# Optimization experiments

Measured on AMD Instinct MI355X. Metric: run time of the kernel, lower is better.

Reference implementation:

```python
import jax, jax.numpy as jnp
import numpy as np

N_NODES = 100000
N_EDGES = 1600000
IN_DIM = 128
N_HID = 128


def setup_inputs() -> dict:
    key = jax.random.key(0)
    k1, k2, k3, k4 = jax.random.split(key, 4)
    node_feature = jax.random.normal(k1, (N_NODES, IN_DIM), dtype=jnp.float32)
    edge_index = jax.random.randint(k2, (2, N_EDGES), 0, N_NODES, dtype=jnp.int64)
    # GCN layer weights (glorot-ish scale)
    W1 = jax.random.normal(k3, (IN_DIM, N_HID), dtype=jnp.float32) / np.sqrt(IN_DIM)
    b1 = jnp.zeros((N_HID,), dtype=jnp.float32)
    W2 = jax.random.normal(k4, (N_HID, N_HID), dtype=jnp.float32) / np.sqrt(N_HID)
    b2 = jnp.zeros((N_HID,), dtype=jnp.float32)
    return {"node_feature": node_feature, "edge_index": edge_index,
            "W1": W1, "b1": b1, "W2": W2, "b2": b2}


def _gcn_layer(x, W, b, row, col, n_nodes):
    """GCNConv: x' = D^-1/2 (A + I) D^-1/2 (x W) + b, symmetric norm with self-loops."""
    xt = x @ W  # [N, out]
    ones = jnp.ones(row.shape[0], dtype=xt.dtype)
    deg = jnp.zeros((n_nodes,), dtype=xt.dtype).at[col].add(ones) + 1.0  # +1 self-loop
    dinv = jax.lax.rsqrt(deg)  # [N]
    norm = dinv[row] * dinv[col]  # [E]
    # gather messages from source (row), scatter-add into destination (col)
    agg = jnp.zeros_like(xt).at[col].add(xt[row] * norm[:, None])
    agg = agg + xt * (dinv * dinv)[:, None]  # self-loop contribution
    return agg + b


def reference(node_feature, edge_index, W1, b1, W2, b2):
    row, col = edge_index[0], edge_index[1]
    n = node_feature.shape[0]
    h = _gcn_layer(node_feature, W1, b1, row, col, n)
    # F.dropout with training=False is identity (eval-mode reference)
    h = _gcn_layer(h, W2, b2, row, col, n)
    return h
```

## Files before the change

### kernel.cpp

```cpp
#include <hip/hip_runtime.h>

typedef unsigned short ushort_t;
typedef __attribute__((ext_vector_type(8))) short short8;
typedef __attribute__((ext_vector_type(8))) unsigned short us8v;
typedef __attribute__((ext_vector_type(4))) float f32x4;

__device__ __forceinline__ float b2f(unsigned short u) {
    union { unsigned int i; float f; } v; v.i = ((unsigned int)u) << 16; return v.f;
}
__device__ __forceinline__ unsigned short f2b(float f) {
    union { float f; unsigned int i; } v; v.f = f;
    unsigned int r = (v.i + 0x7FFF + ((v.i >> 16) & 1)) >> 16;
    return (unsigned short)r;
}

__device__ __forceinline__ void load_edge(const int* __restrict__ ei, int e, int E,
                                          int is64, int& s, int& d) {
    if (is64) { s = ei[2 * e]; d = ei[2 * (E + e)]; }
    else      { s = ei[e];     d = ei[E + e]; }
}

__global__ void k_hist(const int* __restrict__ ei, int E, unsigned N,
                       int* __restrict__ bhist, int BSH, int NB) {
    __shared__ int lh[256];
    int t = threadIdx.x;
    for (int b = t; b < NB; b += 256) lh[b] = 0;
    int z = 0;
    for (int i = t; i < 512; i += 256) z |= ei[2 * i + 1];
    int is64 = (__syncthreads_or(z) == 0);
    int e0 = blockIdx.x * 4096;
    #pragma unroll
    for (int i = 0; i < 16; ++i) {
        int e = e0 + i * 256 + t;
        if (e < E) {
            int s, d; load_edge(ei, e, E, is64, s, d);
            if ((unsigned)s < N && (unsigned)d < N) atomicAdd(&lh[d >> BSH], 1);
        }
    }
    __syncthreads();
    for (int b = t; b < NB; b += 256) { int v = lh[b]; if (v) atomicAdd(&bhist[b], v); }
}

__global__ void k_scanb(const int* __restrict__ bhist, int NB,
                        int* __restrict__ bkbase, int* __restrict__ bkcur) {
    __shared__ int sd[256];
    int t = threadIdx.x;
    int v0 = (t < NB) ? bhist[t] : 0;
    sd[t] = v0;
    for (int o = 1; o < 256; o <<= 1) {
        __syncthreads();
        int v = (t >= o) ? sd[t - o] : 0;
        __syncthreads();
        sd[t] += v;
    }
    __syncthreads();
    if (t < NB) { int ex = sd[t] - v0; bkbase[t] = ex; bkcur[t] = ex; }
}

__global__ __launch_bounds__(256) void k_bucket(const int* __restrict__ ei, int E, unsigned N,
                                                int* __restrict__ bkcur,
                                                int* __restrict__ bs, int* __restrict__ bd,
                                                int BSH, int NB) {
    __shared__ int lss[4096];
    __shared__ int ldd[4096];
    __shared__ int lhist[256];
    __shared__ int lcur[256];
    int t = threadIdx.x;
    int e0 = blockIdx.x * 4096;
    for (int b = t; b < NB; b += 256) lhist[b] = 0;
    int z = 0;
    for (int i = t; i < 512; i += 256) z |= ei[2 * i + 1];
    int is64 = (__syncthreads_or(z) == 0);
    #pragma unroll
    for (int i = 0; i < 16; ++i) {
        int idx = i * 256 + t, e = e0 + idx;
        int s = -1, d = -1;
        if (e < E) {
            load_edge(ei, e, E, is64, s, d);
            if (!((unsigned)s < N && (unsigned)d < N)) d = -1;
        }
        lss[idx] = s; ldd[idx] = d;
        if (d >= 0) atomicAdd(&lhist[d >> BSH], 1);
    }
    __syncthreads();
    for (int b = t; b < NB; b += 256) {
        int v = lhist[b];
        lcur[b] = v ? atomicAdd(&bkcur[b], v) : 0;
    }
    __syncthreads();
    #pragma unroll
    for (int i = 0; i < 16; ++i) {
        int idx = i * 256 + t;
        int d = ldd[idx];
        if (d >= 0) {
            int p = atomicAdd(&lcur[d >> BSH], 1);
            bs[p] = lss[idx]; bd[p] = d;
        }
    }
}

__global__ void k_count2(const int* __restrict__ bd, const int* __restrict__ bkbase,
                         const int* __restrict__ bkcur, int N, int BSH,
                         int* __restrict__ cnt) {
    __shared__ int lc[512];
    int b = blockIdx.x, t = threadIdx.x;
    int nbase = b << BSH;
    int nn = min(1 << BSH, N - nbase);
    for (int j = t; j < nn; j += 256) lc[j] = 0;
    __syncthreads();
    int s0 = bkbase[b], s1 = bkcur[b];
    for (int i = s0 + t; i < s1; i += 256) atomicAdd(&lc[bd[i] - nbase], 1);
    __syncthreads();
    for (int j = t; j < nn; j += 256) cnt[nbase + j] = lc[j];
}

__global__ void k_assign(int* __restrict__ cnt, int N,
                         int* __restrict__ pos, float* __restrict__ dinv,
                         int* __restrict__ cursor, int* __restrict__ srcs,
                         int padidx) {
    __shared__ int sd[256];
    __shared__ int sbase;
    int t = threadIdx.x;
    int n = blockIdx.x * 256 + t;
    int c = (n < N) ? cnt[n] : 0;
    int cp = (c + 7) & ~7;
    sd[t] = cp;
    for (int o = 1; o < 256; o <<= 1) {
        __syncthreads();
        int v = (t >= o) ? sd[t - o] : 0;
        __syncthreads();
        sd[t] += v;
    }
    __syncthreads();
    if (t == 255) sbase = atomicAdd(cursor, sd[255]);
    __syncthreads();
    if (n < N) {
        int st = sbase + sd[t] - cp;
        pos[n] = st;
        dinv[n] = rsqrtf((float)c + 1.0f);
        cnt[n] = cp;
        for (int q = c; q < cp; ++q) srcs[st + q] = padidx;
    }
}

__global__ void k_fill2(const int* __restrict__ bs, const int* __restrict__ bd,
                        const int* __restrict__ bkbase, const int* __restrict__ bkcur,
                        const int* __restrict__ pos, int N, int BSH,
                        int* __restrict__ srcs) {
    __shared__ int lcur[512];
    int b = blockIdx.x, t = threadIdx.x;
    int nbase = b << BSH;
    int nn = min(1 << BSH, N - nbase);
    for (int j = t; j < nn; j += 256) lcur[j] = pos[nbase + j];
    __syncthreads();
    int s0 = bkbase[b], s1 = bkcur[b];
    for (int i = s0 + t; i < s1; i += 256) {
        int d = bd[i];
        int p = atomicAdd(&lcur[d - nbase], 1);
        srcs[p] = bs[i];
    }
}

__global__ void k_transpose(const float* __restrict__ W1, const float* __restrict__ W2,
                            ushort_t* __restrict__ WT, ushort_t* __restrict__ xt,
                            int N) {
    if (blockIdx.x == 2) {
        int t = threadIdx.x;
        if (t < 128) xt[((size_t)N << 7) + t] = 0;
        return;
    }
    const float* src = blockIdx.x ? W2 : W1;
    ushort_t* dst = WT + blockIdx.x * 16384;
    for (int i = threadIdx.x; i < 16384; i += 256) {
        int n = i >> 7, k = i & 127;
        dst[i] = f2b(src[k * 128 + n]);
    }
}

__global__ __launch_bounds__(256) void k_gemm(const float* __restrict__ A,
                                              const ushort_t* __restrict__ WT,
                                              ushort_t* __restrict__ C,
                                              const float* __restrict__ dinv, int M) {
    __shared__ __align__(16) ushort_t sA[64 * 136];
    __shared__ __align__(16) ushort_t sW[128 * 136];
    int t = threadIdx.x;
    int row0 = blockIdx.x * 64;

    #pragma unroll
    for (int it = 0; it < 8; ++it) {
        int flat = (it * 256 + t) * 8;
        int n = flat >> 7, k = flat & 127;
        uint4 v = *(const uint4*)(WT + flat);
        *(uint4*)(&sW[n * 136 + k]) = v;
    }
    #pragma unroll
    for (int it = 0; it < 4; ++it) {
        int flat = (it * 256 + t) * 8;
        int r = flat >> 7, cc = flat & 127;
        int row = row0 + r; if (row > M - 1) row = M - 1;
        const float* p = A + (size_t)row * 128 + cc;
        float4 f0 = *(const float4*)p;
        float4 f1 = *(const float4*)(p + 4);
        ushort_t tmp[8] __attribute__((aligned(16)));
        tmp[0] = f2b(f0.x); tmp[1] = f2b(f0.y); tmp[2] = f2b(f0.z); tmp[3] = f2b(f0.w);
        tmp[4] = f2b(f1.x); tmp[5] = f2b(f1.y); tmp[6] = f2b(f1.z); tmp[7] = f2b(f1.w);
        *(uint4*)(&sA[r * 136 + cc]) = *(const uint4*)tmp;
    }
    __syncthreads();

    int w = t >> 6, lane = t & 63;
    int m = lane & 15, quad = lane >> 4;

    f32x4 acc[8] = {};
    #pragma unroll
    for (int k0 = 0; k0 < 128; k0 += 32) {
        short8 af = *(const short8*)(&sA[(w * 16 + m) * 136 + k0 + quad * 8]);
        #pragma unroll
        for (int tt = 0; tt < 8; ++tt) {
            short8 bf = *(const short8*)(&sW[(tt * 16 + m) * 136 + k0 + quad * 8]);
            acc[tt] = __builtin_amdgcn_mfma_f32_16x16x32_bf16(af, bf, acc[tt], 0, 0, 0);
        }
    }
    #pragma unroll
    for (int r = 0; r < 4; ++r) {
        int row = row0 + w * 16 + quad * 4 + r;
        if (row < M) {
            float dd = dinv[row];
            #pragma unroll
            for (int tt = 0; tt < 8; ++tt)
                C[(size_t)row * 128 + tt * 16 + m] = f2b(dd * acc[tt][r]);
        }
    }
}

__global__ __launch_bounds__(256) void k_agg(const ushort_t* __restrict__ xt,
                                             const float* __restrict__ bias,
                                             float* __restrict__ out,
                                             const int* __restrict__ pos,
                                             const int* __restrict__ cnts,
                                             const float* __restrict__ dinv,
                                             const int* __restrict__ srcs, int N) {
    int lane = threadIdx.x & 63;
    int slot = lane >> 4, j = lane & 15;
    int d = (blockIdx.x << 2) + (threadIdx.x >> 6);
    if (d >= N) return;
    int cn = cnts[d];
    int start = pos[d];
    float dd = dinv[d];
    us8v vs = *(const us8v*)(xt + ((size_t)d << 7) + (j << 3));
    float4 bb0 = *(const float4*)(bias + (j << 3));
    float4 bb1 = *(const float4*)(bias + (j << 3) + 4);

    float a0 = 0.f, a1 = 0.f, a2 = 0.f, a3 = 0.f;
    float a4 = 0.f, a5 = 0.f, a6 = 0.f, a7 = 0.f;

    for (int base = 0; base < cn; base += 64) {
        int n = cn - base; if (n > 64) n = 64;
        int sv = 0;
        if (lane < n) sv = srcs[start + base + lane];
        #pragma unroll 2
        for (int c = 0; c < n; c += 8) {
            int s0 = __shfl(sv, c + slot);
            int s1 = __shfl(sv, c + 4 + slot);
            us8v v0 = *(const us8v*)(xt + ((size_t)s0 << 7) + (j << 3));
            us8v v1 = *(const us8v*)(xt + ((size_t)s1 << 7) + (j << 3));
            a0 += b2f(v0[0]); a1 += b2f(v0[1]); a2 += b2f(v0[2]); a3 += b2f(v0[3]);
            a4 += b2f(v0[4]); a5 += b2f(v0[5]); a6 += b2f(v0[6]); a7 += b2f(v0[7]);
            a0 += b2f(v1[0]); a1 += b2f(v1[1]); a2 += b2f(v1[2]); a3 += b2f(v1[3]);
            a4 += b2f(v1[4]); a5 += b2f(v1[5]); a6 += b2f(v1[6]); a7 += b2f(v1[7]);
        }
    }
    a0 += __shfl_xor(a0, 32); a1 += __shfl_xor(a1, 32);
    a2 += __shfl_xor(a2, 32); a3 += __shfl_xor(a3, 32);
    a4 += __shfl_xor(a4, 32); a5 += __shfl_xor(a5, 32);
    a6 += __shfl_xor(a6, 32); a7 += __shfl_xor(a7, 32);
    a0 += __shfl_xor(a0, 16); a1 += __shfl_xor(a1, 16);
    a2 += __shfl_xor(a2, 16); a3 += __shfl_xor(a3, 16);
    a4 += __shfl_xor(a4, 16); a5 += __shfl_xor(a5, 16);
    a6 += __shfl_xor(a6, 16); a7 += __shfl_xor(a7, 16);

    if (slot == 0) {
        float4 o0, o1;
        o0.x = dd * (a0 + b2f(vs[0])) + bb0.x;
        o0.y = dd * (a1 + b2f(vs[1])) + bb0.y;
        o0.z = dd * (a2 + b2f(vs[2])) + bb0.z;
        o0.w = dd * (a3 + b2f(vs[3])) + bb0.w;
        o1.x = dd * (a4 + b2f(vs[4])) + bb1.x;
        o1.y = dd * (a5 + b2f(vs[5])) + bb1.y;
        o1.z = dd * (a6 + b2f(vs[6])) + bb1.z;
        o1.w = dd * (a7 + b2f(vs[7])) + bb1.w;
        float4* po = (float4*)(out + ((size_t)d << 7) + (j << 3));
        po[0] = o0; po[1] = o1;
    }
}


extern "C" void kernel_launch(void* const* d_in, const int* in_sizes, int n_in,
                              void* d_out, int out_size, void* d_ws, size_t ws_size,
                              hipStream_t stream) {
    const float* x  = (const float*)d_in[0];
    const int*   ei = (const int*)d_in[1];
    const float* W1 = (const float*)d_in[2];
    const float* b1 = (const float*)d_in[3];
    const float* W2 = (const float*)d_in[4];
    const float* b2 = (const float*)d_in[5];
    float* out = (float*)d_out;

    const int N = in_sizes[0] / 128;
    const int E = in_sizes[1] / 2;

    int BSH = 9;
    int NB = (N + (1 << BSH) - 1) >> BSH;
    while (NB > 256) { BSH++; NB = (N + (1 << BSH) - 1) >> BSH; }

    char* ws = (char*)d_ws;
    size_t o = 0;
    auto take = [&](size_t bytes) { size_t r = o; o = (o + bytes + 255) & ~(size_t)255; return r; };
    size_t o_bhist  = take(256 * 4);
    size_t o_cursor = take(4);
    size_t zero_end = o;
    size_t o_bkbase = take(256 * 4);
    size_t o_bkcur  = take(256 * 4);
    size_t o_cnt    = take((size_t)N * 4);
    size_t o_pos    = take((size_t)N * 4);
    size_t o_dinv   = take((size_t)N * 4);
    size_t o_srcs   = take(((size_t)E + 7 * (size_t)N + 64) * 4);
    size_t o_WT     = take(2 * 128 * 128 * 2);
    size_t big_sz   = (size_t)E * 8 > (size_t)(N + 1) * 256 ? (size_t)E * 8
                                                            : (size_t)(N + 1) * 256;
    size_t o_big    = take(big_sz);
    (void)ws_size;

    int*      bhist  = (int*)(ws + o_bhist);
    int*      cursor = (int*)(ws + o_cursor);
    int*      bkbase = (int*)(ws + o_bkbase);
    int*      bkcur  = (int*)(ws + o_bkcur);
    int*      cnt    = (int*)(ws + o_cnt);
    int*      pos    = (int*)(ws + o_pos);
    float*    dinv   = (float*)(ws + o_dinv);
    int*      srcs   = (int*)(ws + o_srcs);
    ushort_t* WT     = (ushort_t*)(ws + o_WT);
    int*      bs     = (int*)(ws + o_big);
    int*      bd     = (int*)(ws + o_big) + E;
    ushort_t* xt     = (ushort_t*)(ws + o_big);
    float*    h      = out;

    hipMemsetAsync(d_ws, 0, zero_end, stream);

    int gE = (E + 4095) / 4096;
    int gN = (N + 255) / 256;
    k_hist<<<gE, 256, 0, stream>>>(ei, E, (unsigned)N, bhist, BSH, NB);
    k_scanb<<<1, 256, 0, stream>>>(bhist, NB, bkbase, bkcur);
    k_bucket<<<gE, 256, 0, stream>>>(ei, E, (unsigned)N, bkcur, bs, bd, BSH, NB);
    k_count2<<<NB, 256, 0, stream>>>(bd, bkbase, bkcur, N, BSH, cnt);
    k_assign<<<gN, 256, 0, stream>>>(cnt, N, pos, dinv, cursor, srcs, N);
    k_fill2<<<NB, 256, 0, stream>>>(bs, bd, bkbase, bkcur, pos, N, BSH, srcs);
    k_transpose<<<3, 256, 0, stream>>>(W1, W2, WT, xt, N);

    int gG = (N + 63) / 64;
    int gA = (N + 3) / 4;
    k_gemm<<<gG, 256, 0, stream>>>(x, WT, xt, dinv, N);
    k_agg<<<gA, 256, 0, stream>>>(xt, b1, h, pos, cnt, dinv, srcs, N);
    k_gemm<<<gG, 256, 0, stream>>>(h, WT + 16384, xt, dinv, N);
    k_agg<<<gA, 256, 0, stream>>>(xt, b2, out, pos, cnt, dinv, srcs, N);
}
```

Measured before the change: 352.5 us.

## Replace bucketed CSR build with direct atomics, store hidden layer as bf16

The two-level bucket sort (histogram, scan, bucket scatter, per-bucket count and fill) becomes a direct global-atomic degree count followed by a global-atomic fill into per-node cursors. This cuts the kernel launches and the intermediate bucket arrays, but adds contended global atomics and random writes. Separately, the first aggregation now writes its hidden output as bf16, which the second GEMM reads directly. That halves the intermediate traffic and drops a conversion in the GEMM. The aggregation loop is also reshaped to software-pipeline its gather loads.

```diff
diff --git a/kernel.cpp b/kernel.cpp
--- a/kernel.cpp
+++ b/kernel.cpp
@@ -16,108 +16,39 @@
 
 __device__ __forceinline__ void load_edge(const int* __restrict__ ei, int e, int E,
                                           int is64, int& s, int& d) {
-    if (is64) { s = ei[2 * e]; d = ei[2 * (E + e)]; }
-    else      { s = ei[e];     d = ei[E + e]; }
-}
-
-__global__ void k_hist(const int* __restrict__ ei, int E, unsigned N,
-                       int* __restrict__ bhist, int BSH, int NB) {
-    __shared__ int lh[256];
-    int t = threadIdx.x;
-    for (int b = t; b < NB; b += 256) lh[b] = 0;
+    if (is64) {
+        const long long* el = (const long long*)ei;
+        s = (int)el[e]; d = (int)el[E + e];
+    } else {
+        s = ei[e]; d = ei[E + e];
+    }
+}
+
+__device__ __forceinline__ int detect64(const int* __restrict__ ei, int t) {
     int z = 0;
     for (int i = t; i < 512; i += 256) z |= ei[2 * i + 1];
-    int is64 = (__syncthreads_or(z) == 0);
+    return (__syncthreads_or(z) == 0);
+}
+
+__global__ void k_count(const int* __restrict__ ei, int E, unsigned N,
+                        int* __restrict__ cnt) {
+    int t = threadIdx.x;
+    int is64 = detect64(ei, t);
     int e0 = blockIdx.x * 4096;
     #pragma unroll
     for (int i = 0; i < 16; ++i) {
         int e = e0 + i * 256 + t;
         if (e < E) {
             int s, d; load_edge(ei, e, E, is64, s, d);
-            if ((unsigned)s < N && (unsigned)d < N) atomicAdd(&lh[d >> BSH], 1);
-        }
-    }
-    __syncthreads();
-    for (int b = t; b < NB; b += 256) { int v = lh[b]; if (v) atomicAdd(&bhist[b], v); }
-}
-
-__global__ void k_scanb(const int* __restrict__ bhist, int NB,
-                        int* __restrict__ bkbase, int* __restrict__ bkcur) {
-    __shared__ int sd[256];
-    int t = threadIdx.x;
-    int v0 = (t < NB) ? bhist[t] : 0;
-    sd[t] = v0;
-    for (int o = 1; o < 256; o <<= 1) {
-        __syncthreads();
-        int v = (t >= o) ? sd[t - o] : 0;
-        __syncthreads();
-        sd[t] += v;
-    }
-    __syncthreads();
-    if (t < NB) { int ex = sd[t] - v0; bkbase[t] = ex; bkcur[t] = ex; }
-}
-
-__global__ __launch_bounds__(256) void k_bucket(const int* __restrict__ ei, int E, unsigned N,
-                                                int* __restrict__ bkcur,
-                                                int* __restrict__ bs, int* __restrict__ bd,
-                                                int BSH, int NB) {
-    __shared__ int lss[4096];
-    __shared__ int ldd[4096];
-    __shared__ int lhist[256];
-    __shared__ int lcur[256];
-    int t = threadIdx.x;
-    int e0 = blockIdx.x * 4096;
-    for (int b = t; b < NB; b += 256) lhist[b] = 0;
-    int z = 0;
-    for (int i = t; i < 512; i += 256) z |= ei[2 * i + 1];
-    int is64 = (__syncthreads_or(z) == 0);
-    #pragma unroll
-    for (int i = 0; i < 16; ++i) {
-        int idx = i * 256 + t, e = e0 + idx;
-        int s = -1, d = -1;
-        if (e < E) {
-            load_edge(ei, e, E, is64, s, d);
-            if (!((unsigned)s < N && (unsigned)d < N)) d = -1;
-        }
-        lss[idx] = s; ldd[idx] = d;
-        if (d >= 0) atomicAdd(&lhist[d >> BSH], 1);
-    }
-    __syncthreads();
-    for (int b = t; b < NB; b += 256) {
-        int v = lhist[b];
-        lcur[b] = v ? atomicAdd(&bkcur[b], v) : 0;
-    }
-    __syncthreads();
-    #pragma unroll
-    for (int i = 0; i < 16; ++i) {
-        int idx = i * 256 + t;
-        int d = ldd[idx];
-        if (d >= 0) {
-            int p = atomicAdd(&lcur[d >> BSH], 1);
-            bs[p] = lss[idx]; bd[p] = d;
-        }
-    }
-}
-
-__global__ void k_count2(const int* __restrict__ bd, const int* __restrict__ bkbase,
-                         const int* __restrict__ bkcur, int N, int BSH,
-                         int* __restrict__ cnt) {
-    __shared__ int lc[512];
-    int b = blockIdx.x, t = threadIdx.x;
-    int nbase = b << BSH;
-    int nn = min(1 << BSH, N - nbase);
-    for (int j = t; j < nn; j += 256) lc[j] = 0;
-    __syncthreads();
-    int s0 = bkbase[b], s1 = bkcur[b];
-    for (int i = s0 + t; i < s1; i += 256) atomicAdd(&lc[bd[i] - nbase], 1);
-    __syncthreads();
-    for (int j = t; j < nn; j += 256) cnt[nbase + j] = lc[j];
+            if ((unsigned)s < N && (unsigned)d < N) atomicAdd(&cnt[d], 1);
+        }
+    }
 }
 
 __global__ void k_assign(int* __restrict__ cnt, int N,
-                         int* __restrict__ pos, float* __restrict__ dinv,
-                         int* __restrict__ cursor, int* __restrict__ srcs,
-                         int padidx) {
+                         int* __restrict__ pos, int* __restrict__ poscur,
+                         float* __restrict__ dinv, int* __restrict__ cursor,
+                         int* __restrict__ srcs, int padidx) {
     __shared__ int sd[256];
     __shared__ int sbase;
     int t = threadIdx.x;
@@ -137,27 +68,28 @@
     if (n < N) {
         int st = sbase + sd[t] - cp;
         pos[n] = st;
+        poscur[n] = st;
         dinv[n] = rsqrtf((float)c + 1.0f);
         cnt[n] = cp;
         for (int q = c; q < cp; ++q) srcs[st + q] = padidx;
     }
 }
 
-__global__ void k_fill2(const int* __restrict__ bs, const int* __restrict__ bd,
-                        const int* __restrict__ bkbase, const int* __restrict__ bkcur,
-                        const int* __restrict__ pos, int N, int BSH,
-                        int* __restrict__ srcs) {
-    __shared__ int lcur[512];
-    int b = blockIdx.x, t = threadIdx.x;
-    int nbase = b << BSH;
-    int nn = min(1 << BSH, N - nbase);
-    for (int j = t; j < nn; j += 256) lcur[j] = pos[nbase + j];
-    __syncthreads();
-    int s0 = bkbase[b], s1 = bkcur[b];
-    for (int i = s0 + t; i < s1; i += 256) {
-        int d = bd[i];
-        int p = atomicAdd(&lcur[d - nbase], 1);
-        srcs[p] = bs[i];
+__global__ void k_fill(const int* __restrict__ ei, int E, unsigned N,
+                       int* __restrict__ poscur, int* __restrict__ srcs) {
+    int t = threadIdx.x;
+    int is64 = detect64(ei, t);
+    int e0 = blockIdx.x * 4096;
+    #pragma unroll
+    for (int i = 0; i < 16; ++i) {
+        int e = e0 + i * 256 + t;
+        if (e < E) {
+            int s, d; load_edge(ei, e, E, is64, s, d);
+            if ((unsigned)s < N && (unsigned)d < N) {
+                int p = atomicAdd(&poscur[d], 1);
+                srcs[p] = s;
+            }
+        }
     }
 }
 
@@ -177,7 +109,8 @@
     }
 }
 
-__global__ __launch_bounds__(256) void k_gemm(const float* __restrict__ A,
+template <bool ABF>
+__global__ __launch_bounds__(256) void k_gemm(const void* __restrict__ Ap,
                                               const ushort_t* __restrict__ WT,
                                               ushort_t* __restrict__ C,
                                               const float* __restrict__ dinv, int M) {
@@ -198,13 +131,20 @@
         int flat = (it * 256 + t) * 8;
         int r = flat >> 7, cc = flat & 127;
         int row = row0 + r; if (row > M - 1) row = M - 1;
-        const float* p = A + (size_t)row * 128 + cc;
-        float4 f0 = *(const float4*)p;
-        float4 f1 = *(const float4*)(p + 4);
-        ushort_t tmp[8] __attribute__((aligned(16)));
-        tmp[0] = f2b(f0.x); tmp[1] = f2b(f0.y); tmp[2] = f2b(f0.z); tmp[3] = f2b(f0.w);
-        tmp[4] = f2b(f1.x); tmp[5] = f2b(f1.y); tmp[6] = f2b(f1.z); tmp[7] = f2b(f1.w);
-        *(uint4*)(&sA[r * 136 + cc]) = *(const uint4*)tmp;
+        if (ABF) {
+            const ushort_t* A = (const ushort_t*)Ap;
+            us8v v = *(const us8v*)(A + ((size_t)row << 7) + cc);
+            *(us8v*)(&sA[r * 136 + cc]) = v;
+        } else {
+            const float* A = (const float*)Ap;
+            const float* p = A + (size_t)row * 128 + cc;
+            float4 f0 = *(const float4*)p;
+            float4 f1 = *(const float4*)(p + 4);
+            ushort_t tmp[8] __attribute__((aligned(16)));
+            tmp[0] = f2b(f0.x); tmp[1] = f2b(f0.y); tmp[2] = f2b(f0.z); tmp[3] = f2b(f0.w);
+            tmp[4] = f2b(f1.x); tmp[5] = f2b(f1.y); tmp[6] = f2b(f1.z); tmp[7] = f2b(f1.w);
+            *(uint4*)(&sA[r * 136 + cc]) = *(const uint4*)tmp;
+        }
     }
     __syncthreads();
 
@@ -233,9 +173,10 @@
     }
 }
 
+template <bool OBF>
 __global__ __launch_bounds__(256) void k_agg(const ushort_t* __restrict__ xt,
                                              const float* __restrict__ bias,
-                                             float* __restrict__ out,
+                                             void* __restrict__ outp,
                                              const int* __restrict__ pos,
                                              const int* __restrict__ cnts,
                                              const float* __restrict__ dinv,
@@ -258,17 +199,25 @@
         int n = cn - base; if (n > 64) n = 64;
         int sv = 0;
         if (lane < n) sv = srcs[start + base + lane];
-        #pragma unroll 2
-        for (int c = 0; c < n; c += 8) {
-            int s0 = __shfl(sv, c + slot);
-            int s1 = __shfl(sv, c + 4 + slot);
-            us8v v0 = *(const us8v*)(xt + ((size_t)s0 << 7) + (j << 3));
-            us8v v1 = *(const us8v*)(xt + ((size_t)s1 << 7) + (j << 3));
+        int s0 = __shfl(sv, slot);
+        int s1 = __shfl(sv, 4 + slot);
+        us8v v0 = *(const us8v*)(xt + ((size_t)s0 << 7) + (j << 3));
+        us8v v1 = *(const us8v*)(xt + ((size_t)s1 << 7) + (j << 3));
+        for (int c = 8; c < n; c += 8) {
+            int t0 = __shfl(sv, c + slot);
+            int t1 = __shfl(sv, c + 4 + slot);
+            us8v w0 = *(const us8v*)(xt + ((size_t)t0 << 7) + (j << 3));
+            us8v w1 = *(const us8v*)(xt + ((size_t)t1 << 7) + (j << 3));
             a0 += b2f(v0[0]); a1 += b2f(v0[1]); a2 += b2f(v0[2]); a3 += b2f(v0[3]);
             a4 += b2f(v0[4]); a5 += b2f(v0[5]); a6 += b2f(v0[6]); a7 += b2f(v0[7]);
             a0 += b2f(v1[0]); a1 += b2f(v1[1]); a2 += b2f(v1[2]); a3 += b2f(v1[3]);
             a4 += b2f(v1[4]); a5 += b2f(v1[5]); a6 += b2f(v1[6]); a7 += b2f(v1[7]);
-        }
+            v0 = w0; v1 = w1;
+        }
+        a0 += b2f(v0[0]); a1 += b2f(v0[1]); a2 += b2f(v0[2]); a3 += b2f(v0[3]);
+        a4 += b2f(v0[4]); a5 += b2f(v0[5]); a6 += b2f(v0[6]); a7 += b2f(v0[7]);
+        a0 += b2f(v1[0]); a1 += b2f(v1[1]); a2 += b2f(v1[2]); a3 += b2f(v1[3]);
+        a4 += b2f(v1[4]); a5 += b2f(v1[5]); a6 += b2f(v1[6]); a7 += b2f(v1[7]);
     }
     a0 += __shfl_xor(a0, 32); a1 += __shfl_xor(a1, 32);
     a2 += __shfl_xor(a2, 32); a3 += __shfl_xor(a3, 32);
@@ -280,17 +229,25 @@
     a6 += __shfl_xor(a6, 16); a7 += __shfl_xor(a7, 16);
 
     if (slot == 0) {
-        float4 o0, o1;
-        o0.x = dd * (a0 + b2f(vs[0])) + bb0.x;
-        o0.y = dd * (a1 + b2f(vs[1])) + bb0.y;
-        o0.z = dd * (a2 + b2f(vs[2])) + bb0.z;
-        o0.w = dd * (a3 + b2f(vs[3])) + bb0.w;
-        o1.x = dd * (a4 + b2f(vs[4])) + bb1.x;
-        o1.y = dd * (a5 + b2f(vs[5])) + bb1.y;
-        o1.z = dd * (a6 + b2f(vs[6])) + bb1.z;
-        o1.w = dd * (a7 + b2f(vs[7])) + bb1.w;
-        float4* po = (float4*)(out + ((size_t)d << 7) + (j << 3));
-        po[0] = o0; po[1] = o1;
+        float o0 = dd * (a0 + b2f(vs[0])) + bb0.x;
+        float o1 = dd * (a1 + b2f(vs[1])) + bb0.y;
+        float o2 = dd * (a2 + b2f(vs[2])) + bb0.z;
+        float o3 = dd * (a3 + b2f(vs[3])) + bb0.w;
+        float o4 = dd * (a4 + b2f(vs[4])) + bb1.x;
+        float o5 = dd * (a5 + b2f(vs[5])) + bb1.y;
+        float o6 = dd * (a6 + b2f(vs[6])) + bb1.z;
+        float o7 = dd * (a7 + b2f(vs[7])) + bb1.w;
+        if (OBF) {
+            ushort_t tmp[8] __attribute__((aligned(16)));
+            tmp[0] = f2b(o0); tmp[1] = f2b(o1); tmp[2] = f2b(o2); tmp[3] = f2b(o3);
+            tmp[4] = f2b(o4); tmp[5] = f2b(o5); tmp[6] = f2b(o6); tmp[7] = f2b(o7);
+            *(us8v*)((ushort_t*)outp + ((size_t)d << 7) + (j << 3)) = *(const us8v*)tmp;
+        } else {
+            float4 q0 = { o0, o1, o2, o3 };
+            float4 q1 = { o4, o5, o6, o7 };
+            float4* po = (float4*)((float*)outp + ((size_t)d << 7) + (j << 3));
+            po[0] = q0; po[1] = q1;
+        }
     }
 }
 
@@ -309,58 +266,44 @@
     const int N = in_sizes[0] / 128;
     const int E = in_sizes[1] / 2;
 
-    int BSH = 9;
-    int NB = (N + (1 << BSH) - 1) >> BSH;
-    while (NB > 256) { BSH++; NB = (N + (1 << BSH) - 1) >> BSH; }
-
     char* ws = (char*)d_ws;
     size_t o = 0;
     auto take = [&](size_t bytes) { size_t r = o; o = (o + bytes + 255) & ~(size_t)255; return r; };
-    size_t o_bhist  = take(256 * 4);
     size_t o_cursor = take(4);
+    size_t o_cnt    = take((size_t)N * 4);
     size_t zero_end = o;
-    size_t o_bkbase = take(256 * 4);
-    size_t o_bkcur  = take(256 * 4);
-    size_t o_cnt    = take((size_t)N * 4);
     size_t o_pos    = take((size_t)N * 4);
+    size_t o_poscur = take((size_t)N * 4);
     size_t o_dinv   = take((size_t)N * 4);
     size_t o_srcs   = take(((size_t)E + 7 * (size_t)N + 64) * 4);
     size_t o_WT     = take(2 * 128 * 128 * 2);
-    size_t big_sz   = (size_t)E * 8 > (size_t)(N + 1) * 256 ? (size_t)E * 8
-                                                            : (size_t)(N + 1) * 256;
-    size_t o_big    = take(big_sz);
+    size_t o_xt     = take((size_t)(N + 1) * 256);
     (void)ws_size;
 
-    int*      bhist  = (int*)(ws + o_bhist);
     int*      cursor = (int*)(ws + o_cursor);
-    int*      bkbase = (int*)(ws + o_bkbase);
-    int*      bkcur  = (int*)(ws + o_bkcur);
     int*      cnt    = (int*)(ws + o_cnt);
     int*      pos    = (int*)(ws + o_pos);
+    int*      poscur = (int*)(ws + o_poscur);
     float*    dinv   = (float*)(ws + o_dinv);
     int*      srcs   = (int*)(ws + o_srcs);
     ushort_t* WT     = (ushort_t*)(ws + o_WT);
-    int*      bs     = (int*)(ws + o_big);
-    int*      bd     = (int*)(ws + o_big) + E;
-    ushort_t* xt     = (ushort_t*)(ws + o_big);
-    float*    h      = out;
+    ushort_t* xt     = (ushort_t*)(ws + o_xt);
+    ushort_t* hbf    = (ushort_t*)d_out;
 
     hipMemsetAsync(d_ws, 0, zero_end, stream);
 
     int gE = (E + 4095) / 4096;
     int gN = (N + 255) / 256;
-    k_hist<<<gE, 256, 0, stream>>>(ei, E, (unsigned)N, bhist, BSH, NB);
-    k_scanb<<<1, 256, 0, stream>>>(bhist, NB, bkbase, bkcur);
-    k_bucket<<<gE, 256, 0, stream>>>(ei, E, (unsigned)N, bkcur, bs, bd, BSH, NB);
-    k_count2<<<NB, 256, 0, stream>>>(bd, bkbase, bkcur, N, BSH, cnt);
-    k_assign<<<gN, 256, 0, stream>>>(cnt, N, pos, dinv, cursor, srcs, N);
-    k_fill2<<<NB, 256, 0, stream>>>(bs, bd, bkbase, bkcur, pos, N, BSH, srcs);
-    k_transpose<<<3, 256, 0, stream>>>(W1, W2, WT, xt, N);
-
     int gG = (N + 63) / 64;
     int gA = (N + 3) / 4;
-    k_gemm<<<gG, 256, 0, stream>>>(x, WT, xt, dinv, N);
-    k_agg<<<gA, 256, 0, stream>>>(xt, b1, h, pos, cnt, dinv, srcs, N);
-    k_gemm<<<gG, 256, 0, stream>>>(h, WT + 16384, xt, dinv, N);
-    k_agg<<<gA, 256, 0, stream>>>(xt, b2, out, pos, cnt, dinv, srcs, N);
-}
+
+    k_count<<<gE, 256, 0, stream>>>(ei, E, (unsigned)N, cnt);
+    k_assign<<<gN, 256, 0, stream>>>(cnt, N, pos, poscur, dinv, cursor, srcs, N);
+    k_fill<<<gE, 256, 0, stream>>>(ei, E, (unsigned)N, poscur, srcs);
+    k_transpose<<<3, 256, 0, stream>>>(W1, W2, WT, xt, N);
+
+    k_gemm<false><<<gG, 256, 0, stream>>>(x, WT, xt, dinv, N);
+    k_agg<true><<<gA, 256, 0, stream>>>(xt, b1, hbf, pos, cnt, dinv, srcs, N);
+    k_gemm<true><<<gG, 256, 0, stream>>>(hbf, WT + 16384, xt, dinv, N);
+    k_agg<false><<<gA, 256, 0, stream>>>(xt, b2, out, pos, cnt, dinv, srcs, N);
+}
```

Measured after the change: 440.9 us. 25.1% more time.
